# Optimization experiments

Hardware: AMD Instinct MI355X
Metric: run time of the kernel (lower is better)

The kernel has to match this reference:

```python
import jax, jax.numpy as jnp
import numpy as np

BATCH, SEQ, IN_DIM = 128, 512, 512
FEATURES, OUT_DIM = 1024, 256


def setup_inputs() -> dict:
    key = jax.random.key(0)
    ks = jax.random.split(key, 7)
    s_i = 1.0 / np.sqrt(IN_DIM)
    s_h = 1.0 / np.sqrt(FEATURES)
    return {
        "inputs": jax.random.normal(ks[0], (BATCH, SEQ, IN_DIM), jnp.float32),
        # input-to-hidden for gates [r, z, n], each Dense has bias in flax GRUCell
        "Wi": jax.random.normal(ks[1], (IN_DIM, 3 * FEATURES), jnp.float32) * s_i,
        "bi": jnp.zeros((3 * FEATURES,), jnp.float32),
        # hidden-to-hidden for [r, z, n]; only the 'n' hidden dense has a bias
        "Wh": jax.random.normal(ks[2], (FEATURES, 3 * FEATURES), jnp.float32) * s_h,
        "bhn": jnp.zeros((FEATURES,), jnp.float32),
        # output head
        "Wo": jax.random.normal(ks[3], (FEATURES, OUT_DIM), jnp.float32) * s_h,
        "bo": jnp.zeros((OUT_DIM,), jnp.float32),
    }


def reference(inputs, Wi, bi, Wh, bhn, Wo, bo):
    B, T, _ = inputs.shape
    F = Wh.shape[0]
    # precompute all input projections in one big GEMM: [B,T,3F]
    xi = jnp.einsum("bti,ig->btg", inputs, Wi) + bi
    x_ir, x_iz, x_in = jnp.split(xi, 3, axis=-1)

    Whr, Whz, Whn = jnp.split(Wh, 3, axis=-1)

    def step(h, xs):
        xr, xz, xn = xs
        r = jax.nn.sigmoid(xr + h @ Whr)
        z = jax.nn.sigmoid(xz + h @ Whz)
        n = jnp.tanh(xn + r * (h @ Whn + bhn))
        h_new = (1.0 - z) * n + z * h
        return h_new, None

    h0 = jnp.zeros((B, F), inputs.dtype)
    # scan over time: [T,B,F] slices
    xs = (jnp.swapaxes(x_ir, 0, 1), jnp.swapaxes(x_iz, 0, 1), jnp.swapaxes(x_in, 0, 1))
    carry, _ = jax.lax.scan(step, h0, xs)
    output = carry @ Wo + bo
    return (output, carry)
```

## Files before the change

kernel.cpp:

```cpp
#include <hip/hip_runtime.h>
#include <hip/hip_bf16.h>
#include <math.h>

#define BATCH 128
#define SEQ   512
#define IND   512
#define F     1024
#define OUTD  256
#define KC    1536
#define N3    3072

typedef __bf16 v8bf __attribute__((ext_vector_type(8)));
typedef float  v4f  __attribute__((ext_vector_type(4)));
typedef unsigned short u16;
typedef u16 v8u __attribute__((ext_vector_type(8)));
typedef unsigned long long u64t;


__device__ inline u16 f2bf(float x) {
    union { float f; unsigned u; } v; v.f = x;
    unsigned r = v.u + 0x7fff + ((v.u >> 16) & 1);
    return (u16)(r >> 16);
}
__device__ inline float bf2f(u16 h) {
    union { unsigned u; float f; } v; v.u = ((unsigned)h) << 16;
    return v.f;
}

__device__ inline float sigm(float x) { return 1.f / (1.f + __expf(-x)); }
__device__ inline float tanh_fast(float x) {
    float xc = fminf(fmaxf(x, -15.f), 15.f);
    float e = __expf(2.f * xc);
    return (e - 1.f) / (e + 1.f);
}

__global__ void k_prep_x(const float* __restrict__ in, u16* __restrict__ xpk) {
    int gid = blockIdx.x * 256 + threadIdx.x;
    int b = gid >> 15;
    int rem = gid & 32767;
    int t = rem >> 6;
    int c = rem & 63;
    const float* s = in + (size_t)gid * 8;
    float4 a0 = ((const float4*)s)[0];
    float4 a1 = ((const float4*)s)[1];
    float a[8] = {a0.x, a0.y, a0.z, a0.w, a1.x, a1.y, a1.z, a1.w};
    v8u oh, ol;
    #pragma unroll
    for (int i = 0; i < 8; i++) {
        u16 h = f2bf(a[i]);
        oh[i] = h;
        ol[i] = f2bf(a[i] - bf2f(h));
    }
    int gb = b >> 5, mt = (b >> 4) & 1, l15 = b & 15;
    int chunk = c >> 2, q = c & 3;
    int lane = q * 16 + l15;
    size_t base = ((size_t)(t * 4 + gb) * 16 + chunk) * 2048 + mt * 512 + lane * 8;
    *(v8u*)(xpk + base) = oh;
    *(v8u*)(xpk + base + 1024) = ol;
}

__global__ void k_prep_w(const float* __restrict__ Wi, const float* __restrict__ Wh,
                         u16* __restrict__ Whi, u16* __restrict__ Wlo) {
    __shared__ float lds[32][33];
    int nb = blockIdx.x % 96;
    int kb = blockIdx.x / 96;
    int tid = threadIdx.x;
    int n_l = tid & 31, kr = tid >> 5;
    #pragma unroll
    for (int j = 0; j < 4; j++) {
        int k_l = kr + j * 8;
        int k = kb * 32 + k_l, n = nb * 32 + n_l;
        float v = (k < F) ? Wh[(size_t)k * N3 + n] : Wi[(size_t)(k - F) * N3 + n];
        lds[k_l][n_l] = v;
    }
    __syncthreads();
    int k_l2 = tid & 31, nr = tid >> 5;
    #pragma unroll
    for (int j = 0; j < 4; j++) {
        int n_l2 = nr + j * 8;
        float v = lds[k_l2][n_l2];
        u16 h = f2bf(v);
        size_t off = (size_t)(nb * 32 + n_l2) * KC + kb * 32 + k_l2;
        Whi[off] = h;
        Wlo[off] = f2bf(v - bf2f(h));
    }
}

template<int G2>
__device__ __forceinline__ void do_chunk(v8bf a0h, v8bf a1h, v8bf a0l, v8bf a1l,
                                         v8bf w0h, v8bf w1h, v8bf w2h,
                                         const u16* wlo, v4f (&acc)[4][2]) {
    v8bf w0l = *(const v8bf*)(wlo);
    v8bf w1l = *(const v8bf*)(wlo + 512);
    v8bf w2l = *(const v8bf*)(wlo + 1024);
    acc[0][0]  = __builtin_amdgcn_mfma_f32_16x16x32_bf16(a0h, w0h, acc[0][0], 0, 0, 0);
    acc[0][1]  = __builtin_amdgcn_mfma_f32_16x16x32_bf16(a1h, w0h, acc[0][1], 0, 0, 0);
    acc[1][0]  = __builtin_amdgcn_mfma_f32_16x16x32_bf16(a0h, w1h, acc[1][0], 0, 0, 0);
    acc[1][1]  = __builtin_amdgcn_mfma_f32_16x16x32_bf16(a1h, w1h, acc[1][1], 0, 0, 0);
    acc[G2][0] = __builtin_amdgcn_mfma_f32_16x16x32_bf16(a0h, w2h, acc[G2][0], 0, 0, 0);
    acc[G2][1] = __builtin_amdgcn_mfma_f32_16x16x32_bf16(a1h, w2h, acc[G2][1], 0, 0, 0);
    acc[0][0]  = __builtin_amdgcn_mfma_f32_16x16x32_bf16(a0h, w0l, acc[0][0], 0, 0, 0);
    acc[0][1]  = __builtin_amdgcn_mfma_f32_16x16x32_bf16(a1h, w0l, acc[0][1], 0, 0, 0);
    acc[1][0]  = __builtin_amdgcn_mfma_f32_16x16x32_bf16(a0h, w1l, acc[1][0], 0, 0, 0);
    acc[1][1]  = __builtin_amdgcn_mfma_f32_16x16x32_bf16(a1h, w1l, acc[1][1], 0, 0, 0);
    acc[G2][0] = __builtin_amdgcn_mfma_f32_16x16x32_bf16(a0h, w2l, acc[G2][0], 0, 0, 0);
    acc[G2][1] = __builtin_amdgcn_mfma_f32_16x16x32_bf16(a1h, w2l, acc[G2][1], 0, 0, 0);
    acc[0][0]  = __builtin_amdgcn_mfma_f32_16x16x32_bf16(a0l, w0h, acc[0][0], 0, 0, 0);
    acc[0][1]  = __builtin_amdgcn_mfma_f32_16x16x32_bf16(a1l, w0h, acc[0][1], 0, 0, 0);
    acc[1][0]  = __builtin_amdgcn_mfma_f32_16x16x32_bf16(a0l, w1h, acc[1][0], 0, 0, 0);
    acc[1][1]  = __builtin_amdgcn_mfma_f32_16x16x32_bf16(a1l, w1h, acc[1][1], 0, 0, 0);
    acc[G2][0] = __builtin_amdgcn_mfma_f32_16x16x32_bf16(a0l, w2h, acc[G2][0], 0, 0, 0);
    acc[G2][1] = __builtin_amdgcn_mfma_f32_16x16x32_bf16(a1l, w2h, acc[G2][1], 0, 0, 0);
}

__device__ __forceinline__ v8bf load_h8(const u16* p) {
    union { u64t d[2]; v8bf v; } u;
    const u64t* q = (const u64t*)p;
    u.d[0] = __hip_atomic_load(q,     __ATOMIC_RELAXED, __HIP_MEMORY_SCOPE_AGENT);
    u.d[1] = __hip_atomic_load(q + 1, __ATOMIC_RELAXED, __HIP_MEMORY_SCOPE_AGENT);
    return u.v;
}

__launch_bounds__(512)
__global__ void k_gru(const u16* __restrict__ xpk,
                      const u16* __restrict__ Whi, const u16* __restrict__ Wlo,
                      u16* __restrict__ hpk,
                      unsigned* __restrict__ pf,
                      const float* __restrict__ bi, const float* __restrict__ bhn,
                      float* __restrict__ dout) {
    __shared__ __align__(16) u16 wloL[73728];
    __shared__ float accL[2304];
    const int tid = threadIdx.x;
    const int w = tid >> 6, l = tid & 63;
    const int gb = blockIdx.x >> 6, gn = blockIdx.x & 63;
    const int l15 = l & 15, q = l >> 4;

    v8bf whx[2][3], whh[4][3];
    #pragma unroll
    for (int j = 0; j < 2; j++)
        #pragma unroll
        for (int g = 0; g < 3; g++) {
            size_t roff = (size_t)(g * F + gn * 16 + l15) * KC + (F + (w * 2 + j) * 32) + q * 8;
            whx[j][g] = *(const v8bf*)(Whi + roff);
            *(v8u*)(&wloL[(((w * 6 + 4 + j) * 3 + g) << 9) + l * 8]) = *(const v8u*)(Wlo + roff);
        }
    #pragma unroll
    for (int j = 0; j < 4; j++)
        #pragma unroll
        for (int g = 0; g < 3; g++) {
            size_t roff = (size_t)(g * F + gn * 16 + l15) * KC + (w * 4 + j) * 32 + q * 8;
            whh[j][g] = *(const v8bf*)(Whi + roff);
            *(v8u*)(&wloL[(((w * 6 + j) * 3 + g) << 9) + l * 8]) = *(const v8u*)(Wlo + roff);
        }
    __syncthreads();

    const int mt_e = (tid >> 7) & 1;
    const int ii   = tid & 127;
    const int rl   = ii >> 3;
    const int cp   = (ii & 7) * 2;
    const int rowg = gb * 32 + mt_e * 16 + rl;
    const int c0g  = gn * 16 + cp;
    float bir0 = 0.f, bir1 = 0.f, biz0 = 0.f, biz1 = 0.f;
    float bin0 = 0.f, bin1 = 0.f, bh0 = 0.f, bh1 = 0.f;
    if (tid < 256) {
        bir0 = bi[c0g];         bir1 = bi[c0g + 1];
        biz0 = bi[F + c0g];     biz1 = bi[F + c0g + 1];
        bin0 = bi[2 * F + c0g]; bin1 = bi[2 * F + c0g + 1];
        bh0  = bhn[c0g];        bh1  = bhn[c0g + 1];
    }
    float hp0 = 0.f, hp1 = 0.f;
    const int st_kk   = c0g >> 5;
    const int st_q    = (c0g >> 3) & 3;
    const int st_e    = c0g & 7;
    const int st_lane = st_q * 16 + rl;
    const size_t st_off = (size_t)gb * 65536 + st_kk * 2048 + mt_e * 512 + st_lane * 8 + st_e;

    for (int t = 0; t < SEQ; t++) {
        v4f acc[4][2];
        #pragma unroll
        for (int gi = 0; gi < 4; gi++)
            #pragma unroll
            for (int mt = 0; mt < 2; mt++) {
                acc[gi][mt][0] = 0.f; acc[gi][mt][1] = 0.f;
                acc[gi][mt][2] = 0.f; acc[gi][mt][3] = 0.f;
            }

        {
            const u16* xb = xpk + (size_t)(t * 4 + gb) * 32768;
            #pragma unroll
            for (int j = 0; j < 2; j++) {
                const u16* cb = xb + (w * 2 + j) * 2048 + l * 8;
                v8bf a0h = *(const v8bf*)(cb);
                v8bf a1h = *(const v8bf*)(cb + 512);
                v8bf a0l = *(const v8bf*)(cb + 1024);
                v8bf a1l = *(const v8bf*)(cb + 1536);
                do_chunk<3>(a0h, a1h, a0l, a1l, whx[j][0], whx[j][1], whx[j][2],
                            &wloL[(((w * 6 + 4 + j) * 3) << 9) + l * 8], acc);
            }
        }

        if (t > 0) {
            {
                const unsigned* fp = pf + gb * 64 + w * 8 + (l & 7);
                unsigned tgt = (unsigned)t;
                long guard = 0;
                for (;;) {
                    unsigned v = __hip_atomic_load(fp, __ATOMIC_RELAXED, __HIP_MEMORY_SCOPE_AGENT);
                    if (__ballot(v < tgt) == 0ull) break;
                    __builtin_amdgcn_s_sleep(1);
                    if (++guard > 4000000L) break;
                }
            }
            asm volatile("" ::: "memory");
            const u16* hs = hpk + (size_t)((t & 1) ^ 1) * 262144 + (size_t)gb * 65536;
            v8bf hA[4], hB[4], hC[4], hD[4];
#define HLOAD(dst, jj) do { const u16* cb = hs + ((w * 4 + (jj)) * 2048) + l * 8; \
            dst[0] = load_h8(cb);        dst[1] = load_h8(cb + 512); \
            dst[2] = load_h8(cb + 1024); dst[3] = load_h8(cb + 1536); } while (0)
            HLOAD(hA, 0); HLOAD(hB, 1); HLOAD(hC, 2); HLOAD(hD, 3);
#define HSTEP(jj, buf) \
            do_chunk<2>(buf[0], buf[1], buf[2], buf[3], \
                        whh[jj][0], whh[jj][1], whh[jj][2], \
                        &wloL[(((w * 6 + (jj)) * 3) << 9) + l * 8], acc)
            HSTEP(0, hA); HSTEP(1, hB); HSTEP(2, hC); HSTEP(3, hD);
#undef HSTEP
#undef HLOAD
        }

#define RED_ONE(S) do { \
            float* p = &accL[(S) * 288 + q * 72 + l15]; \
            if (r == 0) { \
                p[0]  = acc[(S) >> 1][(S) & 1][0]; p[18] = acc[(S) >> 1][(S) & 1][1]; \
                p[36] = acc[(S) >> 1][(S) & 1][2]; p[54] = acc[(S) >> 1][(S) & 1][3]; \
            } else { \
                p[0]  += acc[(S) >> 1][(S) & 1][0]; p[18] += acc[(S) >> 1][(S) & 1][1]; \
                p[36] += acc[(S) >> 1][(S) & 1][2]; p[54] += acc[(S) >> 1][(S) & 1][3]; \
            } } while (0)
        #pragma unroll
        for (int r = 0; r < 8; r++) {
            const int s = (w + r) & 7;
            switch (s) {
                case 0: RED_ONE(0); break;
                case 1: RED_ONE(1); break;
                case 2: RED_ONE(2); break;
                case 3: RED_ONE(3); break;
                case 4: RED_ONE(4); break;
                case 5: RED_ONE(5); break;
                case 6: RED_ONE(6); break;
                case 7: RED_ONE(7); break;
            }
            __syncthreads();
        }
#undef RED_ONE

        if (tid < 256) {
            u16* hd = hpk + (size_t)(t & 1) * 262144;
            int off = rl * 18 + cp;
            float pr0 = accL[(0 * 2 + mt_e) * 288 + off], pr1 = accL[(0 * 2 + mt_e) * 288 + off + 1];
            float pz0 = accL[(1 * 2 + mt_e) * 288 + off], pz1 = accL[(1 * 2 + mt_e) * 288 + off + 1];
            float ph0 = accL[(2 * 2 + mt_e) * 288 + off], ph1 = accL[(2 * 2 + mt_e) * 288 + off + 1];
            float px0 = accL[(3 * 2 + mt_e) * 288 + off], px1 = accL[(3 * 2 + mt_e) * 288 + off + 1];
            float r0 = sigm(pr0 + bir0), r1 = sigm(pr1 + bir1);
            float z0 = sigm(pz0 + biz0), z1 = sigm(pz1 + biz1);
            float n0 = tanh_fast(px0 + bin0 + r0 * (ph0 + bh0));
            float n1 = tanh_fast(px1 + bin1 + r1 * (ph1 + bh1));
            float hn0 = (1.f - z0) * n0 + z0 * hp0;
            float hn1 = (1.f - z1) * n1 + z1 * hp1;
            hp0 = hn0; hp1 = hn1;
            u16 h0 = f2bf(hn0), h1 = f2bf(hn1);
            u16 l0 = f2bf(hn0 - bf2f(h0)), l1 = f2bf(hn1 - bf2f(h1));
            unsigned hipair = (unsigned)h0 | ((unsigned)h1 << 16);
            unsigned lopair = (unsigned)l0 | ((unsigned)l1 << 16);
            __hip_atomic_store((unsigned*)(hd + st_off), hipair,
                               __ATOMIC_RELAXED, __HIP_MEMORY_SCOPE_AGENT);
            __hip_atomic_store((unsigned*)(hd + st_off + 1024), lopair,
                               __ATOMIC_RELAXED, __HIP_MEMORY_SCOPE_AGENT);
            if (t == SEQ - 1) {
                float2 o; o.x = hn0; o.y = hn1;
                *(float2*)(dout + 32768 + (size_t)rowg * F + c0g) = o;
            }
        }
        __threadfence_block();
        __syncthreads();
        if (tid == 0)
            __hip_atomic_store(pf + gb * 64 + gn, (unsigned)(t + 1),
                               __ATOMIC_RELAXED, __HIP_MEMORY_SCOPE_AGENT);
    }
}

__global__ void k_head(const float* __restrict__ hf, const float* __restrict__ Wo,
                       const float* __restrict__ bo, float* __restrict__ dout) {
    int b = blockIdx.x, c = threadIdx.x;
    const float* h = hf + (size_t)b * F;
    float s = bo[c];
    #pragma unroll 4
    for (int k = 0; k < F; k++) s += h[k] * Wo[(size_t)k * OUTD + c];
    dout[(size_t)b * OUTD + c] = s;
}

extern "C" void kernel_launch(void* const* d_in, const int* in_sizes, int n_in,
                              void* d_out, int out_size, void* d_ws, size_t ws_size,
                              hipStream_t stream) {
    const float* inputs = (const float*)d_in[0];
    const float* Wi     = (const float*)d_in[1];
    const float* bi     = (const float*)d_in[2];
    const float* Wh     = (const float*)d_in[3];
    const float* bhn    = (const float*)d_in[4];
    const float* Wo     = (const float*)d_in[5];
    const float* bo     = (const float*)d_in[6];
    float* out = (float*)d_out;

    char* ws = (char*)d_ws;
    u16* xpk = (u16*)ws;
    u16* Whi = (u16*)(ws + 134217728);
    u16* Wlo = (u16*)(ws + 143654912);
    u16* hpk = (u16*)(ws + 153092096);
    unsigned* pf = (unsigned*)(ws + 154140672);

    hipMemsetAsync(pf, 0, 4 * 64 * sizeof(unsigned), stream);

    k_prep_x<<<16384, 256, 0, stream>>>(inputs, xpk);
    k_prep_w<<<4608, 256, 0, stream>>>(Wi, Wh, Whi, Wlo);
    k_gru<<<256, 512, 0, stream>>>(xpk, Whi, Wlo, hpk, pf, bi, bhn, out);
    k_head<<<128, 256, 0, stream>>>(out + (size_t)BATCH * OUTD, Wo, bo, out);
}
```

Before: 3.562 ms.

## Use per-wave progress flags and all-thread gate epilogue to drop trailing barrier

Replaces the single per-block progress flag with eight per-wave flags, so each wave publishes its slice of h without a block-wide __syncthreads at the end of every timestep. The reduction buffer is double-buffered by timestep parity so the next step can start writing partial sums before other waves finish reading. The gate epilogue now runs on all 512 threads with one element each instead of 256 threads with two. One chunk of the low-half input weights moves from LDS into registers. This aims to cut per-step sync latency on the recurrent critical path, at the cost of waiters polling eight times as many flags, 16-bit instead of 32-bit atomic stores of h, and higher register pressure.

```diff
diff --git a/kernel.cpp b/kernel.cpp
--- a/kernel.cpp
+++ b/kernel.cpp
@@ -113,6 +113,31 @@
     acc[G2][1] = __builtin_amdgcn_mfma_f32_16x16x32_bf16(a1l, w2h, acc[G2][1], 0, 0, 0);
 }
 
+template<int G2>
+__device__ __forceinline__ void do_chunk_reg(v8bf a0h, v8bf a1h, v8bf a0l, v8bf a1l,
+                                             v8bf w0h, v8bf w1h, v8bf w2h,
+                                             v8bf w0l, v8bf w1l, v8bf w2l,
+                                             v4f (&acc)[4][2]) {
+    acc[0][0]  = __builtin_amdgcn_mfma_f32_16x16x32_bf16(a0h, w0h, acc[0][0], 0, 0, 0);
+    acc[0][1]  = __builtin_amdgcn_mfma_f32_16x16x32_bf16(a1h, w0h, acc[0][1], 0, 0, 0);
+    acc[1][0]  = __builtin_amdgcn_mfma_f32_16x16x32_bf16(a0h, w1h, acc[1][0], 0, 0, 0);
+    acc[1][1]  = __builtin_amdgcn_mfma_f32_16x16x32_bf16(a1h, w1h, acc[1][1], 0, 0, 0);
+    acc[G2][0] = __builtin_amdgcn_mfma_f32_16x16x32_bf16(a0h, w2h, acc[G2][0], 0, 0, 0);
+    acc[G2][1] = __builtin_amdgcn_mfma_f32_16x16x32_bf16(a1h, w2h, acc[G2][1], 0, 0, 0);
+    acc[0][0]  = __builtin_amdgcn_mfma_f32_16x16x32_bf16(a0h, w0l, acc[0][0], 0, 0, 0);
+    acc[0][1]  = __builtin_amdgcn_mfma_f32_16x16x32_bf16(a1h, w0l, acc[0][1], 0, 0, 0);
+    acc[1][0]  = __builtin_amdgcn_mfma_f32_16x16x32_bf16(a0h, w1l, acc[1][0], 0, 0, 0);
+    acc[1][1]  = __builtin_amdgcn_mfma_f32_16x16x32_bf16(a1h, w1l, acc[1][1], 0, 0, 0);
+    acc[G2][0] = __builtin_amdgcn_mfma_f32_16x16x32_bf16(a0h, w2l, acc[G2][0], 0, 0, 0);
+    acc[G2][1] = __builtin_amdgcn_mfma_f32_16x16x32_bf16(a1h, w2l, acc[G2][1], 0, 0, 0);
+    acc[0][0]  = __builtin_amdgcn_mfma_f32_16x16x32_bf16(a0l, w0h, acc[0][0], 0, 0, 0);
+    acc[0][1]  = __builtin_amdgcn_mfma_f32_16x16x32_bf16(a1l, w0h, acc[0][1], 0, 0, 0);
+    acc[1][0]  = __builtin_amdgcn_mfma_f32_16x16x32_bf16(a0l, w1h, acc[1][0], 0, 0, 0);
+    acc[1][1]  = __builtin_amdgcn_mfma_f32_16x16x32_bf16(a1l, w1h, acc[1][1], 0, 0, 0);
+    acc[G2][0] = __builtin_amdgcn_mfma_f32_16x16x32_bf16(a0l, w2h, acc[G2][0], 0, 0, 0);
+    acc[G2][1] = __builtin_amdgcn_mfma_f32_16x16x32_bf16(a1l, w2h, acc[G2][1], 0, 0, 0);
+}
+
 __device__ __forceinline__ v8bf load_h8(const u16* p) {
     union { u64t d[2]; v8bf v; } u;
     const u64t* q = (const u64t*)p;
@@ -128,21 +153,22 @@
                       unsigned* __restrict__ pf,
                       const float* __restrict__ bi, const float* __restrict__ bhn,
                       float* __restrict__ dout) {
-    __shared__ __align__(16) u16 wloL[73728];
-    __shared__ float accL[2304];
+    __shared__ __align__(16) u16 wloL[61440];
+    __shared__ float accL[4608];
     const int tid = threadIdx.x;
     const int w = tid >> 6, l = tid & 63;
     const int gb = blockIdx.x >> 6, gn = blockIdx.x & 63;
     const int l15 = l & 15, q = l >> 4;
 
-    v8bf whx[2][3], whh[4][3];
+    v8bf whx[2][3], whh[4][3], wlx0[3];
     #pragma unroll
     for (int j = 0; j < 2; j++)
         #pragma unroll
         for (int g = 0; g < 3; g++) {
             size_t roff = (size_t)(g * F + gn * 16 + l15) * KC + (F + (w * 2 + j) * 32) + q * 8;
             whx[j][g] = *(const v8bf*)(Whi + roff);
-            *(v8u*)(&wloL[(((w * 6 + 4 + j) * 3 + g) << 9) + l * 8]) = *(const v8u*)(Wlo + roff);
+            if (j == 0) wlx0[g] = *(const v8bf*)(Wlo + roff);
+            else *(v8u*)(&wloL[(((w * 5 + 4) * 3 + g) << 9) + l * 8]) = *(const v8u*)(Wlo + roff);
         }
     #pragma unroll
     for (int j = 0; j < 4; j++)
@@ -150,30 +176,25 @@
         for (int g = 0; g < 3; g++) {
             size_t roff = (size_t)(g * F + gn * 16 + l15) * KC + (w * 4 + j) * 32 + q * 8;
             whh[j][g] = *(const v8bf*)(Whi + roff);
-            *(v8u*)(&wloL[(((w * 6 + j) * 3 + g) << 9) + l * 8]) = *(const v8u*)(Wlo + roff);
+            *(v8u*)(&wloL[(((w * 5 + j) * 3 + g) << 9) + l * 8]) = *(const v8u*)(Wlo + roff);
         }
     __syncthreads();
 
-    const int mt_e = (tid >> 7) & 1;
-    const int ii   = tid & 127;
-    const int rl   = ii >> 3;
-    const int cp   = (ii & 7) * 2;
-    const int rowg = gb * 32 + mt_e * 16 + rl;
-    const int c0g  = gn * 16 + cp;
-    float bir0 = 0.f, bir1 = 0.f, biz0 = 0.f, biz1 = 0.f;
-    float bin0 = 0.f, bin1 = 0.f, bh0 = 0.f, bh1 = 0.f;
-    if (tid < 256) {
-        bir0 = bi[c0g];         bir1 = bi[c0g + 1];
-        biz0 = bi[F + c0g];     biz1 = bi[F + c0g + 1];
-        bin0 = bi[2 * F + c0g]; bin1 = bi[2 * F + c0g + 1];
-        bh0  = bhn[c0g];        bh1  = bhn[c0g + 1];
-    }
-    float hp0 = 0.f, hp1 = 0.f;
+    const int colL = l & 15;
+    const int rowL = (w & 3) * 4 + (l >> 4);
+    const int mt_e = w >> 2;
+    const int rowg = gb * 32 + mt_e * 16 + rowL;
+    const int c0g  = gn * 16 + colL;
+    const float birC = bi[c0g];
+    const float bizC = bi[F + c0g];
+    const float binC = bi[2 * F + c0g];
+    const float bhC  = bhn[c0g];
+    float hp = 0.f;
     const int st_kk   = c0g >> 5;
     const int st_q    = (c0g >> 3) & 3;
     const int st_e    = c0g & 7;
-    const int st_lane = st_q * 16 + rl;
-    const size_t st_off = (size_t)gb * 65536 + st_kk * 2048 + mt_e * 512 + st_lane * 8 + st_e;
+    const size_t st_off = (size_t)gb * 65536 + st_kk * 2048 + mt_e * 512
+                        + (st_q * 16 + rowL) * 8 + st_e;
 
     for (int t = 0; t < SEQ; t++) {
         v4f acc[4][2];
@@ -187,21 +208,31 @@
 
         {
             const u16* xb = xpk + (size_t)(t * 4 + gb) * 32768;
-            #pragma unroll
-            for (int j = 0; j < 2; j++) {
-                const u16* cb = xb + (w * 2 + j) * 2048 + l * 8;
+            {
+                const u16* cb = xb + (w * 2 + 0) * 2048 + l * 8;
                 v8bf a0h = *(const v8bf*)(cb);
                 v8bf a1h = *(const v8bf*)(cb + 512);
                 v8bf a0l = *(const v8bf*)(cb + 1024);
                 v8bf a1l = *(const v8bf*)(cb + 1536);
-                do_chunk<3>(a0h, a1h, a0l, a1l, whx[j][0], whx[j][1], whx[j][2],
-                            &wloL[(((w * 6 + 4 + j) * 3) << 9) + l * 8], acc);
+                do_chunk_reg<3>(a0h, a1h, a0l, a1l,
+                                whx[0][0], whx[0][1], whx[0][2],
+                                wlx0[0], wlx0[1], wlx0[2], acc);
+            }
+            {
+                const u16* cb = xb + (w * 2 + 1) * 2048 + l * 8;
+                v8bf a0h = *(const v8bf*)(cb);
+                v8bf a1h = *(const v8bf*)(cb + 512);
+                v8bf a0l = *(const v8bf*)(cb + 1024);
+                v8bf a1l = *(const v8bf*)(cb + 1536);
+                do_chunk<3>(a0h, a1h, a0l, a1l,
+                            whx[1][0], whx[1][1], whx[1][2],
+                            &wloL[(((w * 5 + 4) * 3) << 9) + l * 8], acc);
             }
         }
 
         if (t > 0) {
             {
-                const unsigned* fp = pf + gb * 64 + w * 8 + (l & 7);
+                const unsigned* fp = pf + gb * 512 + (w * 8 + (l >> 3)) * 8 + (l & 7);
                 unsigned tgt = (unsigned)t;
                 long guard = 0;
                 for (;;) {
@@ -221,14 +252,15 @@
 #define HSTEP(jj, buf) \
             do_chunk<2>(buf[0], buf[1], buf[2], buf[3], \
                         whh[jj][0], whh[jj][1], whh[jj][2], \
-                        &wloL[(((w * 6 + (jj)) * 3) << 9) + l * 8], acc)
+                        &wloL[(((w * 5 + (jj)) * 3) << 9) + l * 8], acc)
             HSTEP(0, hA); HSTEP(1, hB); HSTEP(2, hC); HSTEP(3, hD);
 #undef HSTEP
 #undef HLOAD
         }
 
+        float* ac = &accL[(t & 1) * 2304];
 #define RED_ONE(S) do { \
-            float* p = &accL[(S) * 288 + q * 72 + l15]; \
+            float* p = ac + (S) * 288 + q * 72 + l15; \
             if (r == 0) { \
                 p[0]  = acc[(S) >> 1][(S) & 1][0]; p[18] = acc[(S) >> 1][(S) & 1][1]; \
                 p[36] = acc[(S) >> 1][(S) & 1][2]; p[54] = acc[(S) >> 1][(S) & 1][3]; \
@@ -253,37 +285,30 @@
         }
 #undef RED_ONE
 
-        if (tid < 256) {
+        {
             u16* hd = hpk + (size_t)(t & 1) * 262144;
-            int off = rl * 18 + cp;
-            float pr0 = accL[(0 * 2 + mt_e) * 288 + off], pr1 = accL[(0 * 2 + mt_e) * 288 + off + 1];
-            float pz0 = accL[(1 * 2 + mt_e) * 288 + off], pz1 = accL[(1 * 2 + mt_e) * 288 + off + 1];
-            float ph0 = accL[(2 * 2 + mt_e) * 288 + off], ph1 = accL[(2 * 2 + mt_e) * 288 + off + 1];
-            float px0 = accL[(3 * 2 + mt_e) * 288 + off], px1 = accL[(3 * 2 + mt_e) * 288 + off + 1];
-            float r0 = sigm(pr0 + bir0), r1 = sigm(pr1 + bir1);
-            float z0 = sigm(pz0 + biz0), z1 = sigm(pz1 + biz1);
-            float n0 = tanh_fast(px0 + bin0 + r0 * (ph0 + bh0));
-            float n1 = tanh_fast(px1 + bin1 + r1 * (ph1 + bh1));
-            float hn0 = (1.f - z0) * n0 + z0 * hp0;
-            float hn1 = (1.f - z1) * n1 + z1 * hp1;
-            hp0 = hn0; hp1 = hn1;
-            u16 h0 = f2bf(hn0), h1 = f2bf(hn1);
-            u16 l0 = f2bf(hn0 - bf2f(h0)), l1 = f2bf(hn1 - bf2f(h1));
-            unsigned hipair = (unsigned)h0 | ((unsigned)h1 << 16);
-            unsigned lopair = (unsigned)l0 | ((unsigned)l1 << 16);
-            __hip_atomic_store((unsigned*)(hd + st_off), hipair,
+            const int off = rowL * 18 + colL;
+            float pr = ac[(0 * 2 + mt_e) * 288 + off];
+            float pz = ac[(1 * 2 + mt_e) * 288 + off];
+            float ph = ac[(2 * 2 + mt_e) * 288 + off];
+            float px = ac[(3 * 2 + mt_e) * 288 + off];
+            float rg = sigm(pr + birC);
+            float zg = sigm(pz + bizC);
+            float ng = tanh_fast(px + binC + rg * (ph + bhC));
+            float hn = (1.f - zg) * ng + zg * hp;
+            hp = hn;
+            u16 hh = f2bf(hn);
+            u16 ll = f2bf(hn - bf2f(hh));
+            __hip_atomic_store(hd + st_off, hh,
                                __ATOMIC_RELAXED, __HIP_MEMORY_SCOPE_AGENT);
-            __hip_atomic_store((unsigned*)(hd + st_off + 1024), lopair,
+            __hip_atomic_store(hd + st_off + 1024, ll,
                                __ATOMIC_RELAXED, __HIP_MEMORY_SCOPE_AGENT);
-            if (t == SEQ - 1) {
-                float2 o; o.x = hn0; o.y = hn1;
-                *(float2*)(dout + 32768 + (size_t)rowg * F + c0g) = o;
-            }
+            if (t == SEQ - 1)
+                dout[32768 + (size_t)rowg * F + c0g] = hn;
         }
         __threadfence_block();
-        __syncthreads();
-        if (tid == 0)
-            __hip_atomic_store(pf + gb * 64 + gn, (unsigned)(t + 1),
+        if (l == 0)
+            __hip_atomic_store(pf + gb * 512 + gn * 8 + w, (unsigned)(t + 1),
                                __ATOMIC_RELAXED, __HIP_MEMORY_SCOPE_AGENT);
     }
 }
@@ -317,7 +342,7 @@
     u16* hpk = (u16*)(ws + 153092096);
     unsigned* pf = (unsigned*)(ws + 154140672);
 
-    hipMemsetAsync(pf, 0, 4 * 64 * sizeof(unsigned), stream);
+    hipMemsetAsync(pf, 0, 4 * 64 * 8 * sizeof(unsigned), stream);
 
     k_prep_x<<<16384, 256, 0, stream>>>(inputs, xpk);
     k_prep_w<<<4608, 256, 0, stream>>>(Wi, Wh, Whi, Wlo);
```

Result: faster. 3.310 ms (-7.1%).
